# Kernel tuning notes

Measured on AMD Instinct MI355X. Metric: run time of the kernel, lower is better.

## Reference

```python
import jax, jax.numpy as jnp
import numpy as np

# 8 directional offsets (dy, dx) for the -1 tap of each 3x3 filter, filter index 0..7
OFFSETS = [(-1, -1), (-1, 0), (-1, 1), (0, -1), (0, 1), (1, -1), (1, 0), (1, 1)]
# pairing used by the original prod(dim=-1): [[0,4],[1,5],[2,6],[3,7]]
PAIRS = np.array([[0, 4], [1, 5], [2, 6], [3, 7]])


def box_mean(x, k):
    """Uniform k x k box-filter mean with zero padding (same as F.conv2d with ones/k^2)."""
    kern = jnp.ones((1, 1, k, k), x.dtype) / (k * k)
    return jax.lax.conv_general_dilated(
        x, kern, window_strides=(1, 1), padding=[(k // 2, k // 2)] * 2,
        dimension_numbers=('NCHW', 'OIHW', 'NCHW'))


def pcm_scale(l, d):
    """Dilated directional diffs (center minus shifted-by-d neighbor, zero pad),
    opposite-pair products, then min over the 4 pairs."""
    b, c, h, w = l.shape
    p = jnp.pad(l, ((0, 0), (0, 0), (d, d), (d, d)))
    # shifted[..., i][y, x] = l[y + dy*d, x + dx*d] (zeros outside)
    shifted = jnp.stack(
        [p[:, :, d + dy * d:d + dy * d + h, d + dx * d:d + dx * d + w]
         for dy, dx in OFFSETS], axis=-1)  # (b,c,h,w,8)
    diff = l[..., None] - shifted          # PCM_i = conv2d(l, filter_i, dilation=d)
    temp = diff[..., PAIRS].prod(axis=-1)  # (b,c,h,w,4)
    return temp.min(axis=-1)               # (b,c,h,w)


def mpcm(x):
    outs = [pcm_scale(box_mean(x, k), k) for k in (3, 5, 7, 9)]
    return jnp.stack(outs, axis=-1).max(axis=-1)


def setup_inputs() -> dict:
    key = jax.random.key(0)
    input_tensor = jax.random.uniform(key, (16, 1, 512, 512), dtype=jnp.float32)
    return {"input_tensor": input_tensor}


def reference(input_tensor):
    out = mpcm(input_tensor)
    # per-image threshold: mean + 3 * unbiased std (torch .std default ddof=1)
    mean = out.mean(axis=(1, 2, 3), keepdims=True)
    std = out.std(axis=(1, 2, 3), keepdims=True, ddof=1)
    th = mean + 3.0 * std
    return (out > th).astype(out.dtype)
```

## Files before the change

kernel.cpp:

```cpp
#include <hip/hip_runtime.h>


namespace {

constexpr int H = 512, W = 512, NIMG = 16;
constexpr int TW = 64, TH = 16;
constexpr int HALO = 13;
constexpr int IR = TH + 2 * HALO + 1;
constexpr int IC = TW + 2 * HALO + 1;
constexpr int WI = IC;
constexpr int NT = 512;
constexpr int LS = 82;

struct Smem {
  union alignas(16) {
    double L[(TH + 18) * LS];
    double red[16];
  } u;
  double I[IR * WI];
};

__device__ __forceinline__ double2 ld2(const double* p) {
  double2 v;
  __builtin_memcpy(&v, p, sizeof(double2));
  return v;
}

template <int K, bool BORDER>
__device__ __forceinline__ void scale_pass(Smem& s, int y0, int x0, double mp[2]) {
  constexpr int R   = K / 2;
  constexpr int LH  = TH + 2 * K;
  constexpr int LW  = TW + 2 * K;
  constexpr int HPW = LW / 2;
  constexpr int NP  = LH * HPW;
  constexpr double inv = 1.0 / (double)(K * K);
  const int tid = threadIdx.x;

  for (int pe = tid; pe < NP; pe += NT) {
    const int yy = pe / HPW;
    const int xx = (pe - yy * HPW) * 2;
    const int li = yy + (HALO - K);
    const int lj = xx + (HALO - K) - R;
    const double* Ia = s.I + (li - R) * WI + lj;
    const double* Ib = Ia + K * WI;
    const double2 a0 = ld2(Ia), aK = ld2(Ia + K);
    const double2 b0 = ld2(Ib), bK = ld2(Ib + K);
    const double s0 = (bK.x - aK.x) - (b0.x - a0.x);
    const double s1 = (bK.y - aK.y) - (b0.y - a0.y);
    double2 o;
    if (BORDER) {
      const int gy = y0 - K + yy, gx = x0 - K + xx;
      const bool in0 = ((unsigned)gy < (unsigned)H) & ((unsigned)gx < (unsigned)W);
      const bool in1 = ((unsigned)gy < (unsigned)H) & ((unsigned)(gx + 1) < (unsigned)W);
      o.x = in0 ? s0 * inv : 0.0;
      o.y = in1 ? s1 * inv : 0.0;
    } else {
      o.x = s0 * inv;
      o.y = s1 * inv;
    }
    *(double2*)&s.u.L[yy * LS + xx] = o;
  }
  __syncthreads();

  {
    const int r  = tid >> 5;
    const int cc = (tid & 31) * 2;
    const double* up  = &s.u.L[r * LS + cc];
    const double* mid = up + K * LS;
    const double* dn  = up + 2 * K * LS;
    const double2 u0 = ld2(up),  uK = ld2(up + K),  u2 = ld2(up + 2 * K);
    const double2 m0 = ld2(mid), mK = ld2(mid + K), m2 = ld2(mid + 2 * K);
    const double2 w0 = ld2(dn),  wK = ld2(dn + K),  w2 = ld2(dn + 2 * K);
    {
      const double c = mK.x;
      const double e0 = c - u0.x, e1 = c - uK.x, e2 = c - u2.x, e3 = c - m0.x;
      const double e4 = c - m2.x, e5 = c - w0.x, e6 = c - wK.x, e7 = c - w2.x;
      const double m = fmin(fmin(e0 * e4, e1 * e5), fmin(e2 * e6, e3 * e7));
      mp[0] = fmax(mp[0], m);
    }
    {
      const double c = mK.y;
      const double e0 = c - u0.y, e1 = c - uK.y, e2 = c - u2.y, e3 = c - m0.y;
      const double e4 = c - m2.y, e5 = c - w0.y, e6 = c - wK.y, e7 = c - w2.y;
      const double m = fmin(fmin(e0 * e4, e1 * e5), fmin(e2 * e6, e3 * e7));
      mp[1] = fmax(mp[1], m);
    }
  }
  __syncthreads();
}

template <bool BORDER>
__device__ __forceinline__ void compute_tile(Smem& s, const float* __restrict__ img,
                                             int y0, int x0, double mp[2]) {
  const int tid = threadIdx.x;
  for (int e = tid; e < IR * IC; e += NT) {
    const int iy = e / IC, ix = e - iy * IC;
    const int gy = y0 - HALO + iy - 1, gx = x0 - HALO + ix - 1;
    double v = 0.0;
    if (BORDER) {
      if (iy > 0 && ix > 0 && (unsigned)gy < (unsigned)H && (unsigned)gx < (unsigned)W)
        v = (double)img[gy * W + gx];
    } else {
      if (iy > 0 && ix > 0) v = (double)img[gy * W + gx];
    }
    s.I[iy * WI + ix] = v;
  }
  __syncthreads();

  if (tid < IR - 1) {
    double* p = &s.I[(tid + 1) * WI + 1];
    double run = 0.0;
#pragma unroll
    for (int x = 0; x < IC - 1; ++x) { run += p[x]; p[x] = run; }
  }
  __syncthreads();

  if (tid < IC - 1) {
    double* p = &s.I[WI + (tid + 1)];
    double run = 0.0;
#pragma unroll
    for (int y = 0; y < IR - 1; ++y) { run += *p; *p = run; p += WI; }
  }
  __syncthreads();

  mp[0] = mp[1] = -1.0e300;
  scale_pass<3, BORDER>(s, y0, x0, mp);
  scale_pass<5, BORDER>(s, y0, x0, mp);
  scale_pass<7, BORDER>(s, y0, x0, mp);
  scale_pass<9, BORDER>(s, y0, x0, mp);
}

__global__ __launch_bounds__(NT, 6) void k_stats(const float* __restrict__ in,
                                                 double* __restrict__ partials,
                                                 double* __restrict__ wsmp) {
  __shared__ Smem s;
  const int img = blockIdx.z;
  const int y0 = blockIdx.y * TH, x0 = blockIdx.x * TW;
  const bool border = (blockIdx.x == 0) | (blockIdx.x == gridDim.x - 1) |
                      (blockIdx.y == 0) | (blockIdx.y == gridDim.y - 1);
  double mp[2];
  if (border) compute_tile<true>(s, in + (size_t)img * H * W, y0, x0, mp);
  else        compute_tile<false>(s, in + (size_t)img * H * W, y0, x0, mp);

  const int tid = threadIdx.x;
  if (wsmp != nullptr) {
    const int r = tid >> 5, cc = (tid & 31) * 2;
    double2 v; v.x = mp[0]; v.y = mp[1];
    *(double2*)&wsmp[(size_t)img * H * W + (size_t)(y0 + r) * W + (x0 + cc)] = v;
  }

  double s1 = mp[0] + mp[1];
  double s2 = mp[0] * mp[0] + mp[1] * mp[1];
#pragma unroll
  for (int off = 32; off; off >>= 1) {
    s1 += __shfl_down(s1, off);
    s2 += __shfl_down(s2, off);
  }
  if ((tid & 63) == 0) { s.u.red[tid >> 6] = s1; s.u.red[8 + (tid >> 6)] = s2; }
  __syncthreads();
  if (tid == 0) {
    double S = 0.0, S2 = 0.0;
#pragma unroll
    for (int w = 0; w < NT / 64; ++w) { S += s.u.red[w]; S2 += s.u.red[8 + w]; }
    const int bl = (img * gridDim.y + blockIdx.y) * gridDim.x + blockIdx.x;
    partials[2 * bl]     = S;
    partials[2 * bl + 1] = S2;
  }
}

__global__ void k_thresh(const double* __restrict__ partials, double* __restrict__ th) {
  const int img = blockIdx.x;
  const int lane = threadIdx.x;
  const int nb = (H / TH) * (W / TW);
  double S = 0.0, S2 = 0.0;
  for (int b = lane; b < nb; b += 64) {
    S  += partials[2 * (img * nb + b)];
    S2 += partials[2 * (img * nb + b) + 1];
  }
#pragma unroll
  for (int off = 32; off; off >>= 1) {
    S  += __shfl_down(S, off);
    S2 += __shfl_down(S2, off);
  }
  if (lane == 0) {
    const double N = (double)(H * W);
    const double mean = S / N;
    double var = (S2 - S * S / N) / (N - 1.0);
    if (var < 0.0) var = 0.0;
    th[img] = mean + 3.0 * sqrt(var);
  }
}

__global__ __launch_bounds__(256) void k_out_cached(const double* __restrict__ wsmp,
                                                    const double* __restrict__ th,
                                                    float* __restrict__ out) {
  const int n = NIMG * H * W / 2;
  for (int i = blockIdx.x * 256 + threadIdx.x; i < n; i += gridDim.x * 256) {
    const double t = th[i >> 17];
    const double2 v = ((const double2*)wsmp)[i];
    float2 o; o.x = (v.x > t) ? 1.0f : 0.0f; o.y = (v.y > t) ? 1.0f : 0.0f;
    ((float2*)out)[i] = o;
  }
}

__global__ __launch_bounds__(NT, 6) void k_out_full(const float* __restrict__ in,
                                                    const double* __restrict__ th,
                                                    float* __restrict__ out) {
  __shared__ Smem s;
  const int img = blockIdx.z;
  const int y0 = blockIdx.y * TH, x0 = blockIdx.x * TW;
  const bool border = (blockIdx.x == 0) | (blockIdx.x == gridDim.x - 1) |
                      (blockIdx.y == 0) | (blockIdx.y == gridDim.y - 1);
  double mp[2];
  if (border) compute_tile<true>(s, in + (size_t)img * H * W, y0, x0, mp);
  else        compute_tile<false>(s, in + (size_t)img * H * W, y0, x0, mp);
  const double t = th[img];
  const int tid = threadIdx.x;
  const int r = tid >> 5, cc = (tid & 31) * 2;
  float2 o;
  o.x = (mp[0] > t) ? 1.0f : 0.0f;
  o.y = (mp[1] > t) ? 1.0f : 0.0f;
  *(float2*)&out[(size_t)img * H * W + (size_t)(y0 + r) * W + (x0 + cc)] = o;
}

}

extern "C" void kernel_launch(void* const* d_in, const int* in_sizes, int n_in,
                              void* d_out, int out_size, void* d_ws, size_t ws_size,
                              hipStream_t stream) {
  const float* in = (const float*)d_in[0];
  float* out = (float*)d_out;

  double* th = (double*)d_ws;
  double* partials = (double*)((char*)d_ws + 4096);
  double* wsmp = (double*)((char*)d_ws + 131072);
  const bool cache = ws_size >= (size_t)131072 + (size_t)NIMG * H * W * 8;

  dim3 grid(W / TW, H / TH, NIMG);
  k_stats<<<grid, NT, 0, stream>>>(in, partials, cache ? wsmp : nullptr);
  k_thresh<<<NIMG, 64, 0, stream>>>(partials, th);
  if (cache) {
    k_out_cached<<<2048, 256, 0, stream>>>(wsmp, th, out);
  } else {
    k_out_full<<<grid, NT, 0, stream>>>(in, th, out);
  }
}
```

Baseline: 105.2 us.

## Double tile height with 1024-thread blocks, unroll staging loops, defer box-mean scaling

Doubles the tile height to 32 rows and the block size to 1024 threads, so the 13-pixel halo is amortised over more output rows and fewer blocks are launched. The staging and box-sum loops become fully unrolled with incremental index stepping, which removes per-element integer divisions. The 1/K^2 box normalisation moves out of the box-sum pass and is applied once to the pair-product minimum as 1/K^4. Larger blocks raise shared memory per block and register pressure under the changed launch bounds, which may lower occupancy. Scaling after the products also changes floating-point rounding slightly.

Result: faster. 91.08 us (-13.4%).

```diff
diff --git a/kernel.cpp b/kernel.cpp
--- a/kernel.cpp
+++ b/kernel.cpp
@@ -4,18 +4,18 @@
 namespace {
 
 constexpr int H = 512, W = 512, NIMG = 16;
-constexpr int TW = 64, TH = 16;
+constexpr int TW = 64, TH = 32;
 constexpr int HALO = 13;
 constexpr int IR = TH + 2 * HALO + 1;
 constexpr int IC = TW + 2 * HALO + 1;
 constexpr int WI = IC;
-constexpr int NT = 512;
+constexpr int NT = 1024;
 constexpr int LS = 82;
 
 struct Smem {
   union alignas(16) {
     double L[(TH + 18) * LS];
-    double red[16];
+    double red[32];
   } u;
   double I[IR * WI];
 };
@@ -33,36 +33,45 @@
   constexpr int LW  = TW + 2 * K;
   constexpr int HPW = LW / 2;
   constexpr int NP  = LH * HPW;
-  constexpr double inv = 1.0 / (double)(K * K);
-  const int tid = threadIdx.x;
-
-  for (int pe = tid; pe < NP; pe += NT) {
-    const int yy = pe / HPW;
-    const int xx = (pe - yy * HPW) * 2;
-    const int li = yy + (HALO - K);
-    const int lj = xx + (HALO - K) - R;
-    const double* Ia = s.I + (li - R) * WI + lj;
-    const double* Ib = Ia + K * WI;
-    const double2 a0 = ld2(Ia), aK = ld2(Ia + K);
-    const double2 b0 = ld2(Ib), bK = ld2(Ib + K);
-    const double s0 = (bK.x - aK.x) - (b0.x - a0.x);
-    const double s1 = (bK.y - aK.y) - (b0.y - a0.y);
-    double2 o;
-    if (BORDER) {
-      const int gy = y0 - K + yy, gx = x0 - K + xx;
-      const bool in0 = ((unsigned)gy < (unsigned)H) & ((unsigned)gx < (unsigned)W);
-      const bool in1 = ((unsigned)gy < (unsigned)H) & ((unsigned)(gx + 1) < (unsigned)W);
-      o.x = in0 ? s0 * inv : 0.0;
-      o.y = in1 ? s1 * inv : 0.0;
-    } else {
-      o.x = s0 * inv;
-      o.y = s1 * inv;
-    }
-    *(double2*)&s.u.L[yy * LS + xx] = o;
+  constexpr int ITERS = (NP + NT - 1) / NT;
+  constexpr int DY  = NT / HPW;
+  constexpr int DX  = NT % HPW;
+  const int tid = threadIdx.x;
+
+  int yy = tid / HPW;
+  int xp = tid - yy * HPW;
+#pragma unroll
+  for (int it = 0; it < ITERS; ++it) {
+    if (yy < LH) {
+      const int xx = xp * 2;
+      const int li = yy + (HALO - K);
+      const int lj = xx + (HALO - K) - R;
+      const double* Ia = s.I + (li - R) * WI + lj;
+      const double* Ib = Ia + K * WI;
+      const double2 a0 = ld2(Ia), aK = ld2(Ia + K);
+      const double2 b0 = ld2(Ib), bK = ld2(Ib + K);
+      const double s0 = (bK.x - aK.x) - (b0.x - a0.x);
+      const double s1 = (bK.y - aK.y) - (b0.y - a0.y);
+      double2 o;
+      if (BORDER) {
+        const int gy = y0 - K + yy, gx = x0 - K + xx;
+        const bool in0 = ((unsigned)gy < (unsigned)H) & ((unsigned)gx < (unsigned)W);
+        const bool in1 = ((unsigned)gy < (unsigned)H) & ((unsigned)(gx + 1) < (unsigned)W);
+        o.x = in0 ? s0 : 0.0;
+        o.y = in1 ? s1 : 0.0;
+      } else {
+        o.x = s0;
+        o.y = s1;
+      }
+      *(double2*)&s.u.L[yy * LS + xx] = o;
+    }
+    xp += DX; yy += DY;
+    if (xp >= HPW) { xp -= HPW; ++yy; }
   }
   __syncthreads();
 
   {
+    constexpr double inv2 = 1.0 / ((double)K * K * K * K);
     const int r  = tid >> 5;
     const int cc = (tid & 31) * 2;
     const double* up  = &s.u.L[r * LS + cc];
@@ -76,14 +85,14 @@
       const double e0 = c - u0.x, e1 = c - uK.x, e2 = c - u2.x, e3 = c - m0.x;
       const double e4 = c - m2.x, e5 = c - w0.x, e6 = c - wK.x, e7 = c - w2.x;
       const double m = fmin(fmin(e0 * e4, e1 * e5), fmin(e2 * e6, e3 * e7));
-      mp[0] = fmax(mp[0], m);
+      mp[0] = fmax(mp[0], m * inv2);
     }
     {
       const double c = mK.y;
       const double e0 = c - u0.y, e1 = c - uK.y, e2 = c - u2.y, e3 = c - m0.y;
       const double e4 = c - m2.y, e5 = c - w0.y, e6 = c - wK.y, e7 = c - w2.y;
       const double m = fmin(fmin(e0 * e4, e1 * e5), fmin(e2 * e6, e3 * e7));
-      mp[1] = fmax(mp[1], m);
+      mp[1] = fmax(mp[1], m * inv2);
     }
   }
   __syncthreads();
@@ -93,17 +102,28 @@
 __device__ __forceinline__ void compute_tile(Smem& s, const float* __restrict__ img,
                                              int y0, int x0, double mp[2]) {
   const int tid = threadIdx.x;
-  for (int e = tid; e < IR * IC; e += NT) {
-    const int iy = e / IC, ix = e - iy * IC;
-    const int gy = y0 - HALO + iy - 1, gx = x0 - HALO + ix - 1;
-    double v = 0.0;
-    if (BORDER) {
-      if (iy > 0 && ix > 0 && (unsigned)gy < (unsigned)H && (unsigned)gx < (unsigned)W)
-        v = (double)img[gy * W + gx];
-    } else {
-      if (iy > 0 && ix > 0) v = (double)img[gy * W + gx];
-    }
-    s.I[iy * WI + ix] = v;
+  {
+    constexpr int NE = IR * IC;
+    constexpr int SITERS = (NE + NT - 1) / NT;
+    constexpr int DIY = NT / IC, DIX = NT % IC;
+    int iy = tid / IC;
+    int ix = tid - iy * IC;
+#pragma unroll
+    for (int it = 0; it < SITERS; ++it) {
+      if (iy < IR) {
+        const int gy = y0 - HALO + iy - 1, gx = x0 - HALO + ix - 1;
+        double v = 0.0;
+        if (BORDER) {
+          if (iy > 0 && ix > 0 && (unsigned)gy < (unsigned)H && (unsigned)gx < (unsigned)W)
+            v = (double)img[gy * W + gx];
+        } else {
+          if (iy > 0 && ix > 0) v = (double)img[gy * W + gx];
+        }
+        s.I[iy * WI + ix] = v;
+      }
+      ix += DIX; iy += DIY;
+      if (ix >= IC) { ix -= IC; ++iy; }
+    }
   }
   __syncthreads();
 
@@ -130,7 +150,7 @@
   scale_pass<9, BORDER>(s, y0, x0, mp);
 }
 
-__global__ __launch_bounds__(NT, 6) void k_stats(const float* __restrict__ in,
+__global__ __launch_bounds__(NT, 8) void k_stats(const float* __restrict__ in,
                                                  double* __restrict__ partials,
                                                  double* __restrict__ wsmp) {
   __shared__ Smem s;
@@ -143,8 +163,8 @@
   else        compute_tile<false>(s, in + (size_t)img * H * W, y0, x0, mp);
 
   const int tid = threadIdx.x;
+  const int r = tid >> 5, cc = (tid & 31) * 2;
   if (wsmp != nullptr) {
-    const int r = tid >> 5, cc = (tid & 31) * 2;
     double2 v; v.x = mp[0]; v.y = mp[1];
     *(double2*)&wsmp[(size_t)img * H * W + (size_t)(y0 + r) * W + (x0 + cc)] = v;
   }
@@ -156,12 +176,12 @@
     s1 += __shfl_down(s1, off);
     s2 += __shfl_down(s2, off);
   }
-  if ((tid & 63) == 0) { s.u.red[tid >> 6] = s1; s.u.red[8 + (tid >> 6)] = s2; }
+  if ((tid & 63) == 0) { s.u.red[tid >> 6] = s1; s.u.red[16 + (tid >> 6)] = s2; }
   __syncthreads();
   if (tid == 0) {
     double S = 0.0, S2 = 0.0;
 #pragma unroll
-    for (int w = 0; w < NT / 64; ++w) { S += s.u.red[w]; S2 += s.u.red[8 + w]; }
+    for (int w = 0; w < NT / 64; ++w) { S += s.u.red[w]; S2 += s.u.red[16 + w]; }
     const int bl = (img * gridDim.y + blockIdx.y) * gridDim.x + blockIdx.x;
     partials[2 * bl]     = S;
     partials[2 * bl + 1] = S2;
@@ -203,7 +223,7 @@
   }
 }
 
-__global__ __launch_bounds__(NT, 6) void k_out_full(const float* __restrict__ in,
+__global__ __launch_bounds__(NT, 8) void k_out_full(const float* __restrict__ in,
                                                     const double* __restrict__ th,
                                                     float* __restrict__ out) {
   __shared__ Smem s;
```
